# Optimization experiments

Measured on AMD Instinct MI355X. Metric: run time of the kernel, lower is better.

The kernel has to match this reference:

```python
import jax, jax.numpy as jnp
import numpy as np
import math

B, H, S, DK = 4, 16, 2048, 64

def setup_inputs() -> dict:
    key = jax.random.key(0)
    kq, kk, kv, km = jax.random.split(key, 4)
    q = jax.random.normal(kq, (B, H, S, DK), dtype=jnp.float32)
    k = jax.random.normal(kk, (B, H, S, DK), dtype=jnp.float32)
    v = jax.random.normal(kv, (B, H, S, DK), dtype=jnp.float32)
    mask = jax.random.randint(km, (B, 1, 1, S), 0, 2, dtype=jnp.int32)
    return {"q": q, "k": k, "v": v, "mask": mask}

def reference(q, k, v, mask):
    scale = 1.0 / math.sqrt(DK)
    # scores: [B, H, S, S]
    scores = jnp.einsum('bhqd,bhkd->bhqk', q, k) * scale
    scores = jnp.where(mask == 0, jnp.float32(-1e9), scores)
    attn = jax.nn.softmax(scores, axis=-1)
    out = jnp.einsum('bhqk,bhkd->bhqd', attn, v)
    return out
```

## Files before the change

kernel.cpp:

```cpp
#include <hip/hip_runtime.h>
#include <hip/hip_bf16.h>

#define S_LEN 2048
#define D_K   64
#define N_H   16
#define N_B   4
#define KVB   64
#define QPB   256
#define NQB   (S_LEN / QPB)
#define NBH   (N_B * N_H)
#define WS_NEED (2L * NBH * S_LEN * D_K * 2 + 4L * S_LEN * 4 + 16)

typedef __attribute__((ext_vector_type(8)))  short bf16x8;
typedef __attribute__((ext_vector_type(16))) float f32x16;
typedef unsigned int u32;
typedef __attribute__((ext_vector_type(4))) u32 u32x4;

__device__ inline short f2bfs(float x) {
    __hip_bfloat16 h = __float2bfloat16(x);
    return __builtin_bit_cast(short, h);
}

__device__ inline bf16x8 cvt8(const float* __restrict__ p) {
    float4 a = *(const float4*)p;
    float4 b = *(const float4*)(p + 4);
    bf16x8 f;
    f[0] = f2bfs(a.x); f[1] = f2bfs(a.y);
    f[2] = f2bfs(a.z); f[3] = f2bfs(a.w);
    f[4] = f2bfs(b.x); f[5] = f2bfs(b.y);
    f[6] = f2bfs(b.z); f[7] = f2bfs(b.w);
    return f;
}

__device__ inline bf16x8 cvt8s(const float* __restrict__ p, float s) {
    float4 a = *(const float4*)p;
    float4 b = *(const float4*)(p + 4);
    bf16x8 f;
    f[0] = f2bfs(a.x * s); f[1] = f2bfs(a.y * s);
    f[2] = f2bfs(a.z * s); f[3] = f2bfs(a.w * s);
    f[4] = f2bfs(b.x * s); f[5] = f2bfs(b.y * s);
    f[6] = f2bfs(b.z * s); f[7] = f2bfs(b.w * s);
    return f;
}

__device__ inline int vswz(int d) { return ((d & 7) ^ ((d >> 3) & 7)) << 4; }

__device__ inline void gld16(const void* g, void* l) {
    __builtin_amdgcn_global_load_lds(
        (const __attribute__((address_space(1))) void*)g,
        (__attribute__((address_space(3))) void*)l, 16, 0, 0);
}

__global__ __launch_bounds__(256)
void gather_cvt(const float* __restrict__ k, const float* __restrict__ v,
                const int* __restrict__ mask, const int dummy,
                short* __restrict__ kc, short* __restrict__ vt,
                int* __restrict__ cnt) {
    const int bid = blockIdx.x, bh = bid >> 5, i0 = (bid & 31) * 64;
    const int b = bh >> 4;
    const int t = threadIdx.x;

    __shared__ __align__(16) short tile_[64][72];
    __shared__ int idx_s[64];
    __shared__ int m_s;

    if (t < 64) {
        const int lane = t;
        const int* mb = mask + b * S_LEN;
        int base = 0;
#pragma unroll 4
        for (int j0 = 0; j0 < S_LEN; j0 += 64) {
            int mv = mb[j0 + lane];
            unsigned long long ball = __ballot(mv != 0);
            int pos = base + __popcll(ball & ((1ull << lane) - 1ull));
            if (mv && pos >= i0 && pos < i0 + 64) idx_s[pos - i0] = j0 + lane;
            base += __popcll(ball);
        }
        if (lane == 0) m_s = base;
    }
    __syncthreads();
    const int m = m_s;
    if (t == 0 && i0 == 0) cnt[b] = m;
    if (i0 >= ((m + 63) & ~63)) return;

    const int r = t >> 2, c0 = (t & 3) * 16;
    const int i = i0 + r;

    bf16x8 fv0, fv1, fk0, fk1;
    if (i < m) {
        const int src = idx_s[r];
        const float* kp = k + ((long)bh * S_LEN + src) * D_K + c0;
        const float* vp = v + ((long)bh * S_LEN + src) * D_K + c0;
        fk0 = cvt8(kp); fk1 = cvt8(kp + 8);
        fv0 = cvt8(vp); fv1 = cvt8(vp + 8);
    } else {
#pragma unroll
        for (int j = 0; j < 8; ++j) { fk0[j] = 0; fk1[j] = 0; fv0[j] = 0; fv1[j] = 0; }
    }
    short* kdst = kc + ((long)bh * S_LEN + i) * D_K + c0;
    *(bf16x8*)kdst       = fk0;
    *(bf16x8*)(kdst + 8) = fk1;
    *(bf16x8*)&tile_[r][c0]     = fv0;
    *(bf16x8*)&tile_[r][c0 + 8] = fv1;
    __syncthreads();
    const int dd = t >> 2, k0 = (t & 3) * 16;
    bf16x8 h0, h1;
#pragma unroll
    for (int j = 0; j < 8; ++j) {
        h0[j] = tile_[k0 + j][dd];
        h1[j] = tile_[k0 + 8 + j][dd];
    }
    short* dst = vt + ((long)bh * D_K + dd) * S_LEN + i0 + k0;
    *(bf16x8*)dst       = h0;
    *(bf16x8*)(dst + 8) = h1;
}

__global__ __launch_bounds__(512)
void attn_fwd(const float* __restrict__ q, const short* __restrict__ kbf,
              const short* __restrict__ vtb, const int* __restrict__ cnt,
              float* __restrict__ out) {
    const int id      = blockIdx.x;
    const int logical = (id & 7) * 64 + (id >> 3);
    const int bh      = logical >> 3;
    const int qblk    = logical & 7;
    const int b       = bh >> 4;
    const int t       = threadIdx.x;
    const int lane    = t & 63;
    const int wq      = t >> 6;
    const int hb      = lane >> 5;
    const int ql      = lane & 31;

    const int m   = cnt[b];
    const int NTr = (m + 63) >> 6;

    __shared__ __align__(16) short kbuf[5][KVB * D_K];
    __shared__ __align__(16) short vbuf[4][D_K * KVB];

    const float scale2 = 0.125f * 1.44269504f;
    const long  baseq  = (long)bh * S_LEN * D_K;
    const int   qrow0  = qblk * QPB + wq * 32;

    bf16x8 qf[4];
    {
        const float* qp = q + baseq + (long)(qrow0 + ql) * D_K + hb * 8;
#pragma unroll
        for (int kd = 0; kd < 4; ++kd) qf[kd] = cvt8s(qp + kd * 16, scale2);
    }

    const int lrow = lane >> 3, lchk = lane & 7;
    const int rA = wq * 8 + lrow;
    const short* ksA = kbf + baseq + (long)rA * D_K + ((lchk ^ (rA & 7)) * 8);
    const short* vsA = vtb + ((long)bh * D_K + rA) * S_LEN
                       + ((lchk ^ ((rA & 7) ^ ((rA >> 3) & 7))) * 8);

    auto STAGE_K = [&](int i) {
        gld16(ksA + (long)i * (KVB * D_K),
              (char*)kbuf + (i % 5) * (KVB * D_K * 2) + (wq * 8) * 128);
    };
    auto STAGE_V = [&](int i) {
        gld16(vsA + (long)i * KVB,
              (char*)vbuf + (i % 4) * (D_K * KVB * 2) + (wq * 8) * 128);
    };

    f32x16 o0, o1;
#pragma unroll
    for (int r = 0; r < 16; ++r) { o0[r] = 0.f; o1[r] = 0.f; }
    float lpart = 0.f;

    f32x16 ZEROV;
#pragma unroll
    for (int r = 0; r < 16; ++r) ZEROV[r] = 0.f;

    f32x16 st0, st1;

    auto QK = [&](int kv0, int sel, bool lastt) {
        const char* kbp = (const char*)kbuf + sel * (KVB * D_K * 2);
        int rb0 = (ql) * 128,      sz0 = (ql & 7) << 4;
        int rb1 = (32 + ql) * 128;
        f32x16 a0, a1;
        __builtin_amdgcn_s_setprio(1);
        {
            int co = (hb * 8) * 2;
            bf16x8 kf0 = *(const bf16x8*)(kbp + ((rb0 + co) ^ sz0));
            bf16x8 kf1 = *(const bf16x8*)(kbp + ((rb1 + co) ^ sz0));
            if (!lastt) {
                a0 = __builtin_amdgcn_mfma_f32_32x32x16_bf16(kf0, qf[0], ZEROV, 0, 0, 0);
                a1 = __builtin_amdgcn_mfma_f32_32x32x16_bf16(kf1, qf[0], ZEROV, 0, 0, 0);
            } else {
                f32x16 c0, c1;
                int keyb = kv0 + 4 * hb;
#pragma unroll
                for (int r = 0; r < 16; ++r) {
                    int key = keyb + (r & 3) + 8 * (r >> 2);
                    c0[r] = (key < m)      ? 0.f : -1e9f;
                    c1[r] = (key + 32 < m) ? 0.f : -1e9f;
                }
                a0 = __builtin_amdgcn_mfma_f32_32x32x16_bf16(kf0, qf[0], c0, 0, 0, 0);
                a1 = __builtin_amdgcn_mfma_f32_32x32x16_bf16(kf1, qf[0], c1, 0, 0, 0);
            }
        }
#pragma unroll
        for (int kd = 1; kd < 4; ++kd) {
            int co = (kd * 16 + hb * 8) * 2;
            bf16x8 kf0 = *(const bf16x8*)(kbp + ((rb0 + co) ^ sz0));
            bf16x8 kf1 = *(const bf16x8*)(kbp + ((rb1 + co) ^ sz0));
            a0 = __builtin_amdgcn_mfma_f32_32x32x16_bf16(kf0, qf[kd], a0, 0, 0, 0);
            a1 = __builtin_amdgcn_mfma_f32_32x32x16_bf16(kf1, qf[kd], a1, 0, 0, 0);
        }
        __builtin_amdgcn_s_setprio(0);
        st0 = a0; st1 = a1;
    };

    u32 w[2][8];

    auto SM = [&]() {
        float rs0 = 0.f, rs1 = 0.f;
#pragma unroll
        for (int mm = 0; mm < 8; ++mm) {
            float p0 = __builtin_amdgcn_exp2f(st0[2 * mm]);
            float p1 = __builtin_amdgcn_exp2f(st0[2 * mm + 1]);
            rs0 += p0; rs1 += p1;
            u32 r;
            asm("v_cvt_pk_bf16_f32 %0, %1, %2" : "=v"(r) : "v"(p0), "v"(p1));
            w[0][mm] = r;
        }
#pragma unroll
        for (int mm = 0; mm < 8; ++mm) {
            float p0 = __builtin_amdgcn_exp2f(st1[2 * mm]);
            float p1 = __builtin_amdgcn_exp2f(st1[2 * mm + 1]);
            rs0 += p0; rs1 += p1;
            u32 r;
            asm("v_cvt_pk_bf16_f32 %0, %1, %2" : "=v"(r) : "v"(p0), "v"(p1));
            w[1][mm] = r;
        }
        lpart += rs0 + rs1;
    };

    auto PV = [&](int sel) {
        const char* vbp = (const char*)vbuf + sel * (D_K * KVB * 2);
#pragma unroll
        for (int kbi = 0; kbi < 4; ++kbi) {
            int c = kbi >> 1, a2 = (kbi & 1) * 4;
            u32 x0 = w[c][a2 + 0], y0 = w[c][a2 + 2];
            u32 x1 = w[c][a2 + 1], y1 = w[c][a2 + 3];
            asm("v_permlane32_swap_b32 %0, %1" : "+v"(x0), "+v"(y0));
            asm("v_permlane32_swap_b32 %0, %1" : "+v"(x1), "+v"(y1));
            u32x4 av = {x0, x1, y0, y1};
            bf16x8 pa = __builtin_bit_cast(bf16x8, av);
            __builtin_amdgcn_s_setprio(1);
#pragma unroll
            for (int dn = 0; dn < 2; ++dn) {
                int d = dn * 32 + ql;
                bf16x8 vf = *(const bf16x8*)(vbp +
                              ((d * 128 + (kbi * 16 + hb * 8) * 2) ^ vswz(d)));
                if (dn == 0)
                    o0 = __builtin_amdgcn_mfma_f32_32x32x16_bf16(pa, vf, o0, 0, 0, 0);
                else
                    o1 = __builtin_amdgcn_mfma_f32_32x32x16_bf16(pa, vf, o1, 0, 0, 0);
            }
            __builtin_amdgcn_s_setprio(0);
        }
    };

    STAGE_K(0);
    STAGE_V(0);
    if (NTr > 1) { STAGE_K(1); STAGE_V(1); }
    if (NTr > 2) STAGE_K(2);
    if (NTr > 3) STAGE_K(3);
    __syncthreads();
    QK(0, 0, NTr == 1);
    __syncthreads();

    for (int u = 0; 2 * u < NTr; ++u) {
        const int t0 = 2 * u, t1 = 2 * u + 1;
        if (t0 + 4 < NTr) STAGE_K(t0 + 4);
        if (t0 + 5 < NTr) STAGE_K(t0 + 5);
        if (t0 + 2 < NTr) STAGE_V(t0 + 2);
        if (t0 + 3 < NTr) STAGE_V(t0 + 3);

        SM();
        if (t0 + 1 < NTr) QK((t0 + 1) * KVB, (t0 + 1) % 5, t0 + 2 == NTr);
        PV(t0 & 3);

        if (t1 < NTr) {
            SM();
            if (t1 + 1 < NTr) QK((t1 + 1) * KVB, (t1 + 1) % 5, t1 + 2 == NTr);
            PV(t1 & 3);
        }

        __syncthreads();
    }

    float lrun = lpart + __shfl_xor(lpart, 32, 64);
    float rl = 1.0f / lrun;
#pragma unroll
    for (int r = 0; r < 16; ++r) {
        int   cr  = (r & 3) + 8 * (r >> 2) + 4 * hb;
        float rlr = __shfl(rl, cr, 64);
        long  rowb = baseq + (long)(qrow0 + cr) * D_K;
        out[rowb + ql]      = o0[r] * rlr;
        out[rowb + 32 + ql] = o1[r] * rlr;
    }
}

__global__ __launch_bounds__(256)
void attn_fwd_legacy(const float* __restrict__ q, const float* __restrict__ k,
                     const float* __restrict__ v, const int* __restrict__ mask,
                     float* __restrict__ out) {
    const int id      = blockIdx.x;
    const int logical = (id & 7) * 128 + (id >> 3);
    const int bh      = logical >> 4;
    const int qblk    = logical & 15;
    const int b       = bh >> 4;
    const int t       = threadIdx.x;
    const int lane    = t & 63;
    const int wq      = t >> 6;
    const int hb      = lane >> 5;
    const int ql      = lane & 31;

    __shared__ __align__(16) short kbuf[KVB * D_K];
    __shared__ __align__(16) short vtbuf[D_K * KVB];
    __shared__ float mbias[S_LEN];

    const float scale2 = 0.125f * 1.44269504f;
    const long  base   = (long)bh * S_LEN * D_K;
    const int   qrow0  = qblk * 128 + wq * 32;

    {
        const int* mb = mask + b * S_LEN;
        for (int i = t; i < S_LEN; i += 256)
            mbias[i] = mb[i] ? 0.f : -1.442695e9f;
    }

    bf16x8 qf[4];
    {
        const float* qp = q + base + (long)(qrow0 + ql) * D_K + hb * 8;
#pragma unroll
        for (int kd = 0; kd < 4; ++kd) qf[kd] = cvt8s(qp + kd * 16, 1.0f);
    }

    f32x16 o0, o1;
#pragma unroll
    for (int r = 0; r < 16; ++r) { o0[r] = 0.f; o1[r] = 0.f; }
    float mrun = -1e30f, lrun = 0.f;

    const int srow = t >> 3;
    const int scol = t & 7;
    float4 kr[2][2], vr[2][2];

    auto LOADT = [&](int kv0) {
#pragma unroll
        for (int u2 = 0; u2 < 2; ++u2) {
            int row = srow + u2 * 32;
            const float* kp = k + base + (long)(kv0 + row) * D_K + scol * 8;
            const float* vp = v + base + (long)(kv0 + row) * D_K + scol * 8;
            kr[u2][0] = *(const float4*)kp; kr[u2][1] = *(const float4*)(kp + 4);
            vr[u2][0] = *(const float4*)vp; vr[u2][1] = *(const float4*)(vp + 4);
        }
    };

    LOADT(0);

    for (int tt = 0; tt < S_LEN / KVB; ++tt) {
        const int kv0 = tt * KVB;
        __syncthreads();
#pragma unroll
        for (int u2 = 0; u2 < 2; ++u2) {
            int row = srow + u2 * 32;
            bf16x8 fk, fv;
#pragma unroll
            for (int j = 0; j < 4; ++j) {
                fk[j]     = f2bfs(((const float*)&kr[u2][0])[j]);
                fk[j + 4] = f2bfs(((const float*)&kr[u2][1])[j]);
                fv[j]     = f2bfs(((const float*)&vr[u2][0])[j]);
                fv[j + 4] = f2bfs(((const float*)&vr[u2][1])[j]);
            }
            int kbyte = (row * 128 + scol * 16) ^ ((row & 7) << 4);
            *(bf16x8*)((char*)kbuf + kbyte) = fk;
#pragma unroll
            for (int j = 0; j < 8; ++j) {
                int d = scol * 8 + j;
                *(short*)((char*)vtbuf + ((d * 128 + row * 2) ^ vswz(d))) = fv[j];
            }
        }
        if (tt + 1 < S_LEN / KVB) LOADT(kv0 + KVB);
        __syncthreads();

        f32x16 stl[2];
#pragma unroll
        for (int kb32 = 0; kb32 < 2; ++kb32) {
            f32x16 acc;
#pragma unroll
            for (int r = 0; r < 16; ++r) acc[r] = 0.f;
            int krow = kb32 * 32 + ql;
            int rb = krow * 128, sz = (krow & 7) << 4;
#pragma unroll
            for (int kd = 0; kd < 4; ++kd) {
                bf16x8 kf = *(const bf16x8*)((const char*)kbuf + ((rb + (kd * 16 + hb * 8) * 2) ^ sz));
                acc = __builtin_amdgcn_mfma_f32_32x32x16_bf16(kf, qf[kd], acc, 0, 0, 0);
            }
            stl[kb32] = acc;
        }
#pragma unroll
        for (int kb32 = 0; kb32 < 2; ++kb32)
#pragma unroll
            for (int r = 0; r < 16; ++r) {
                int key = kv0 + kb32 * 32 + (r & 3) + 8 * (r >> 2) + 4 * hb;
                stl[kb32][r] = fmaf(stl[kb32][r], scale2, mbias[key]);
            }

        float m8[8];
#pragma unroll
        for (int i = 0; i < 8; ++i)
            m8[i] = fmaxf(fmaxf(stl[0][i], stl[0][i + 8]),
                          fmaxf(stl[1][i], stl[1][i + 8]));
        float tmax = fmaxf(fmaxf(fmaxf(m8[0], m8[1]), fmaxf(m8[2], m8[3])),
                           fmaxf(fmaxf(m8[4], m8[5]), fmaxf(m8[6], m8[7])));
        tmax = fmaxf(tmax, __shfl_xor(tmax, 32, 64));

        if (__any(tmax > mrun + 10.0f)) {
            float mnew = fmaxf(mrun, tmax);
            float al   = __builtin_amdgcn_exp2f(mrun - mnew);
            mrun = mnew;
            lrun *= al;
#pragma unroll
            for (int r = 0; r < 16; ++r) {
                float ar = __shfl(al, (r & 3) + 8 * (r >> 2) + 4 * hb, 64);
                o0[r] *= ar; o1[r] *= ar;
            }
        }

        u32 w[2][8];
        float rs = 0.f;
#pragma unroll
        for (int kb32 = 0; kb32 < 2; ++kb32)
#pragma unroll
            for (int mm = 0; mm < 8; ++mm) {
                float p0 = __builtin_amdgcn_exp2f(stl[kb32][2 * mm]     - mrun);
                float p1 = __builtin_amdgcn_exp2f(stl[kb32][2 * mm + 1] - mrun);
                rs += p0 + p1;
                w[kb32][mm] = (u32)(unsigned short)f2bfs(p0) |
                              ((u32)(unsigned short)f2bfs(p1) << 16);
            }
        rs += __shfl_xor(rs, 32, 64);
        lrun += rs;

#pragma unroll
        for (int kbi = 0; kbi < 4; ++kbi) {
            int c = kbi >> 1, a2 = (kbi & 1) * 4;
            u32 x0 = w[c][a2 + 0], y0 = w[c][a2 + 2];
            u32 x1 = w[c][a2 + 1], y1 = w[c][a2 + 3];
            asm("v_permlane32_swap_b32 %0, %1" : "+v"(x0), "+v"(y0));
            asm("v_permlane32_swap_b32 %0, %1" : "+v"(x1), "+v"(y1));
            u32x4 av = {x0, x1, y0, y1};
            bf16x8 pa = __builtin_bit_cast(bf16x8, av);
#pragma unroll
            for (int dn = 0; dn < 2; ++dn) {
                int d = dn * 32 + ql;
                bf16x8 vf = *(const bf16x8*)((const char*)vtbuf +
                              ((d * 128 + (kbi * 16 + hb * 8) * 2) ^ vswz(d)));
                if (dn == 0)
                    o0 = __builtin_amdgcn_mfma_f32_32x32x16_bf16(pa, vf, o0, 0, 0, 0);
                else
                    o1 = __builtin_amdgcn_mfma_f32_32x32x16_bf16(pa, vf, o1, 0, 0, 0);
            }
        }
    }

    float rl = 1.0f / lrun;
#pragma unroll
    for (int r = 0; r < 16; ++r) {
        int   cr  = (r & 3) + 8 * (r >> 2) + 4 * hb;
        float rlr = __shfl(rl, cr, 64);
        long  rowb = base + (long)(qrow0 + cr) * D_K;
        out[rowb + ql]      = o0[r] * rlr;
        out[rowb + 32 + ql] = o1[r] * rlr;
    }
}

extern "C" void kernel_launch(void* const* d_in, const int* in_sizes, int n_in,
                              void* d_out, int out_size, void* d_ws, size_t ws_size,
                              hipStream_t stream) {
    const float* q    = (const float*)d_in[0];
    const float* k    = (const float*)d_in[1];
    const float* v    = (const float*)d_in[2];
    const int*   mask = (const int*)d_in[3];
    float*       out  = (float*)d_out;

    if (ws_size >= (size_t)WS_NEED) {
        short* kc  = (short*)d_ws;
        short* vt  = kc + (long)NBH * S_LEN * D_K;
        int*   cnt = (int*)(vt + (long)NBH * S_LEN * D_K);
        gather_cvt<<<dim3(NBH * (S_LEN / 64)), 256, 0, stream>>>(k, v, mask, 0, kc, vt, cnt);
        attn_fwd<<<dim3(NQB * NBH), 512, 0, stream>>>(q, kc, vt, cnt, out);
    } else {
        attn_fwd_legacy<<<dim3((S_LEN / 128) * NBH), 256, 0, stream>>>(q, k, v, mask, out);
    }
}
```

Measured before the change: 77.60 us.

## Replace LDS-staged K/V pipeline with single-wave blocks loading K/V directly into registers

Each attention block is now a single 64-lane wave handling 32 query rows. K and V tiles are loaded straight from global memory into registers, replacing the shared-memory staging done with global_load_lds, the multi-buffer ring and __syncthreads. The next tile's loads are issued after the current QK and PV. This removes LDS traffic and barriers, but each wave now reads K/V from global or L2 itself, with no sharing across the 8 waves of a block, so global memory traffic rises by about 8x. Latency hiding now depends on occupancy and only one tile of register prefetch.

```diff
diff --git a/kernel.cpp b/kernel.cpp
--- a/kernel.cpp
+++ b/kernel.cpp
@@ -6,8 +6,6 @@
 #define N_H   16
 #define N_B   4
 #define KVB   64
-#define QPB   256
-#define NQB   (S_LEN / QPB)
 #define NBH   (N_B * N_H)
 #define WS_NEED (2L * NBH * S_LEN * D_K * 2 + 4L * S_LEN * 4 + 16)
 
@@ -44,12 +42,6 @@
 }
 
 __device__ inline int vswz(int d) { return ((d & 7) ^ ((d >> 3) & 7)) << 4; }
-
-__device__ inline void gld16(const void* g, void* l) {
-    __builtin_amdgcn_global_load_lds(
-        (const __attribute__((address_space(1))) void*)g,
-        (__attribute__((address_space(3))) void*)l, 16, 0, 0);
-}
 
 __global__ __launch_bounds__(256)
 void gather_cvt(const float* __restrict__ k, const float* __restrict__ v,
@@ -115,30 +107,25 @@
     *(bf16x8*)(dst + 8) = h1;
 }
 
-__global__ __launch_bounds__(512)
+__global__ __launch_bounds__(64)
 void attn_fwd(const float* __restrict__ q, const short* __restrict__ kbf,
               const short* __restrict__ vtb, const int* __restrict__ cnt,
               float* __restrict__ out) {
     const int id      = blockIdx.x;
-    const int logical = (id & 7) * 64 + (id >> 3);
-    const int bh      = logical >> 3;
-    const int qblk    = logical & 7;
+    const int logical = (id & 7) * 512 + (id >> 3);
+    const int bh      = logical >> 6;
+    const int qw      = logical & 63;
     const int b       = bh >> 4;
-    const int t       = threadIdx.x;
-    const int lane    = t & 63;
-    const int wq      = t >> 6;
+    const int lane    = threadIdx.x;
     const int hb      = lane >> 5;
     const int ql      = lane & 31;
 
     const int m   = cnt[b];
     const int NTr = (m + 63) >> 6;
 
-    __shared__ __align__(16) short kbuf[5][KVB * D_K];
-    __shared__ __align__(16) short vbuf[4][D_K * KVB];
-
     const float scale2 = 0.125f * 1.44269504f;
     const long  baseq  = (long)bh * S_LEN * D_K;
-    const int   qrow0  = qblk * QPB + wq * 32;
+    const int   qrow0  = qw * 32;
 
     bf16x8 qf[4];
     {
@@ -147,19 +134,25 @@
         for (int kd = 0; kd < 4; ++kd) qf[kd] = cvt8s(qp + kd * 16, scale2);
     }
 
-    const int lrow = lane >> 3, lchk = lane & 7;
-    const int rA = wq * 8 + lrow;
-    const short* ksA = kbf + baseq + (long)rA * D_K + ((lchk ^ (rA & 7)) * 8);
-    const short* vsA = vtb + ((long)bh * D_K + rA) * S_LEN
-                       + ((lchk ^ ((rA & 7) ^ ((rA >> 3) & 7))) * 8);
-
-    auto STAGE_K = [&](int i) {
-        gld16(ksA + (long)i * (KVB * D_K),
-              (char*)kbuf + (i % 5) * (KVB * D_K * 2) + (wq * 8) * 128);
-    };
-    auto STAGE_V = [&](int i) {
-        gld16(vsA + (long)i * KVB,
-              (char*)vbuf + (i % 4) * (D_K * KVB * 2) + (wq * 8) * 128);
+    const short* kbase = kbf + baseq + (long)ql * D_K + hb * 8;
+    const short* vbase = vtb + ((long)bh * D_K + ql) * S_LEN + hb * 8;
+
+    bf16x8 kc_[8], vc_[8];
+    auto KLOAD = [&](int tile) {
+        const short* p = kbase + (long)tile * (KVB * D_K);
+#pragma unroll
+        for (int kd = 0; kd < 4; ++kd) {
+            kc_[2 * kd + 0] = *(const bf16x8*)(p + kd * 16);
+            kc_[2 * kd + 1] = *(const bf16x8*)(p + 32 * D_K + kd * 16);
+        }
+    };
+    auto VLOAD = [&](int tile) {
+        const short* p = vbase + tile * KVB;
+#pragma unroll
+        for (int kbi = 0; kbi < 4; ++kbi) {
+            vc_[2 * kbi + 0] = *(const bf16x8*)(p + kbi * 16);
+            vc_[2 * kbi + 1] = *(const bf16x8*)(p + 32 * S_LEN + kbi * 16);
+        }
     };
 
     f32x16 o0, o1;
@@ -173,19 +166,13 @@
 
     f32x16 st0, st1;
 
-    auto QK = [&](int kv0, int sel, bool lastt) {
-        const char* kbp = (const char*)kbuf + sel * (KVB * D_K * 2);
-        int rb0 = (ql) * 128,      sz0 = (ql & 7) << 4;
-        int rb1 = (32 + ql) * 128;
+    auto QK = [&](int kv0, bool lastt) {
         f32x16 a0, a1;
         __builtin_amdgcn_s_setprio(1);
         {
-            int co = (hb * 8) * 2;
-            bf16x8 kf0 = *(const bf16x8*)(kbp + ((rb0 + co) ^ sz0));
-            bf16x8 kf1 = *(const bf16x8*)(kbp + ((rb1 + co) ^ sz0));
             if (!lastt) {
-                a0 = __builtin_amdgcn_mfma_f32_32x32x16_bf16(kf0, qf[0], ZEROV, 0, 0, 0);
-                a1 = __builtin_amdgcn_mfma_f32_32x32x16_bf16(kf1, qf[0], ZEROV, 0, 0, 0);
+                a0 = __builtin_amdgcn_mfma_f32_32x32x16_bf16(kc_[0], qf[0], ZEROV, 0, 0, 0);
+                a1 = __builtin_amdgcn_mfma_f32_32x32x16_bf16(kc_[1], qf[0], ZEROV, 0, 0, 0);
             } else {
                 f32x16 c0, c1;
                 int keyb = kv0 + 4 * hb;
@@ -195,17 +182,14 @@
                     c0[r] = (key < m)      ? 0.f : -1e9f;
                     c1[r] = (key + 32 < m) ? 0.f : -1e9f;
                 }
-                a0 = __builtin_amdgcn_mfma_f32_32x32x16_bf16(kf0, qf[0], c0, 0, 0, 0);
-                a1 = __builtin_amdgcn_mfma_f32_32x32x16_bf16(kf1, qf[0], c1, 0, 0, 0);
+                a0 = __builtin_amdgcn_mfma_f32_32x32x16_bf16(kc_[0], qf[0], c0, 0, 0, 0);
+                a1 = __builtin_amdgcn_mfma_f32_32x32x16_bf16(kc_[1], qf[0], c1, 0, 0, 0);
             }
         }
 #pragma unroll
         for (int kd = 1; kd < 4; ++kd) {
-            int co = (kd * 16 + hb * 8) * 2;
-            bf16x8 kf0 = *(const bf16x8*)(kbp + ((rb0 + co) ^ sz0));
-            bf16x8 kf1 = *(const bf16x8*)(kbp + ((rb1 + co) ^ sz0));
-            a0 = __builtin_amdgcn_mfma_f32_32x32x16_bf16(kf0, qf[kd], a0, 0, 0, 0);
-            a1 = __builtin_amdgcn_mfma_f32_32x32x16_bf16(kf1, qf[kd], a1, 0, 0, 0);
+            a0 = __builtin_amdgcn_mfma_f32_32x32x16_bf16(kc_[2 * kd + 0], qf[kd], a0, 0, 0, 0);
+            a1 = __builtin_amdgcn_mfma_f32_32x32x16_bf16(kc_[2 * kd + 1], qf[kd], a1, 0, 0, 0);
         }
         __builtin_amdgcn_s_setprio(0);
         st0 = a0; st1 = a1;
@@ -214,7 +198,7 @@
     u32 w[2][8];
 
     auto SM = [&]() {
-        float rs0 = 0.f, rs1 = 0.f;
+        float rs0 = 0.f, rs1 = 0.f, rs2 = 0.f, rs3 = 0.f;
 #pragma unroll
         for (int mm = 0; mm < 8; ++mm) {
             float p0 = __builtin_amdgcn_exp2f(st0[2 * mm]);
@@ -228,16 +212,15 @@
         for (int mm = 0; mm < 8; ++mm) {
             float p0 = __builtin_amdgcn_exp2f(st1[2 * mm]);
             float p1 = __builtin_amdgcn_exp2f(st1[2 * mm + 1]);
-            rs0 += p0; rs1 += p1;
+            rs2 += p0; rs3 += p1;
             u32 r;
             asm("v_cvt_pk_bf16_f32 %0, %1, %2" : "=v"(r) : "v"(p0), "v"(p1));
             w[1][mm] = r;
         }
-        lpart += rs0 + rs1;
-    };
-
-    auto PV = [&](int sel) {
-        const char* vbp = (const char*)vbuf + sel * (D_K * KVB * 2);
+        lpart += (rs0 + rs1) + (rs2 + rs3);
+    };
+
+    auto PV = [&]() {
 #pragma unroll
         for (int kbi = 0; kbi < 4; ++kbi) {
             int c = kbi >> 1, a2 = (kbi & 1) * 4;
@@ -248,47 +231,21 @@
             u32x4 av = {x0, x1, y0, y1};
             bf16x8 pa = __builtin_bit_cast(bf16x8, av);
             __builtin_amdgcn_s_setprio(1);
-#pragma unroll
-            for (int dn = 0; dn < 2; ++dn) {
-                int d = dn * 32 + ql;
-                bf16x8 vf = *(const bf16x8*)(vbp +
-                              ((d * 128 + (kbi * 16 + hb * 8) * 2) ^ vswz(d)));
-                if (dn == 0)
-                    o0 = __builtin_amdgcn_mfma_f32_32x32x16_bf16(pa, vf, o0, 0, 0, 0);
-                else
-                    o1 = __builtin_amdgcn_mfma_f32_32x32x16_bf16(pa, vf, o1, 0, 0, 0);
-            }
+            o0 = __builtin_amdgcn_mfma_f32_32x32x16_bf16(pa, vc_[2 * kbi + 0], o0, 0, 0, 0);
+            o1 = __builtin_amdgcn_mfma_f32_32x32x16_bf16(pa, vc_[2 * kbi + 1], o1, 0, 0, 0);
             __builtin_amdgcn_s_setprio(0);
         }
     };
 
-    STAGE_K(0);
-    STAGE_V(0);
-    if (NTr > 1) { STAGE_K(1); STAGE_V(1); }
-    if (NTr > 2) STAGE_K(2);
-    if (NTr > 3) STAGE_K(3);
-    __syncthreads();
-    QK(0, 0, NTr == 1);
-    __syncthreads();
-
-    for (int u = 0; 2 * u < NTr; ++u) {
-        const int t0 = 2 * u, t1 = 2 * u + 1;
-        if (t0 + 4 < NTr) STAGE_K(t0 + 4);
-        if (t0 + 5 < NTr) STAGE_K(t0 + 5);
-        if (t0 + 2 < NTr) STAGE_V(t0 + 2);
-        if (t0 + 3 < NTr) STAGE_V(t0 + 3);
-
+    KLOAD(0);
+    VLOAD(0);
+
+    for (int tt = 0; tt < NTr; ++tt) {
+        QK(tt * KVB, tt + 1 == NTr);
+        if (tt + 1 < NTr) KLOAD(tt + 1);
         SM();
-        if (t0 + 1 < NTr) QK((t0 + 1) * KVB, (t0 + 1) % 5, t0 + 2 == NTr);
-        PV(t0 & 3);
-
-        if (t1 < NTr) {
-            SM();
-            if (t1 + 1 < NTr) QK((t1 + 1) * KVB, (t1 + 1) % 5, t1 + 2 == NTr);
-            PV(t1 & 3);
-        }
-
-        __syncthreads();
+        PV();
+        if (tt + 1 < NTr) VLOAD(tt + 1);
     }
 
     float lrun = lpart + __shfl_xor(lpart, 32, 64);
@@ -492,7 +449,7 @@
         short* vt  = kc + (long)NBH * S_LEN * D_K;
         int*   cnt = (int*)(vt + (long)NBH * S_LEN * D_K);
         gather_cvt<<<dim3(NBH * (S_LEN / 64)), 256, 0, stream>>>(k, v, mask, 0, kc, vt, cnt);
-        attn_fwd<<<dim3(NQB * NBH), 512, 0, stream>>>(q, kc, vt, cnt, out);
+        attn_fwd<<<dim3((S_LEN / 32) * NBH), 64, 0, stream>>>(q, kc, vt, cnt, out);
     } else {
         attn_fwd_legacy<<<dim3((S_LEN / 128) * NBH), 256, 0, stream>>>(q, k, v, mask, out);
     }
```

After: 154.8 us. +99.5%, slower.
